# Performance work log

Hardware: AMD Instinct MI355X
Metric: run time of the kernel (lower is better)

Reference implementation:

```python
import jax, jax.numpy as jnp
import numpy as np

N, E, D, H, G, OUT = 50000, 800000, 128, 128, 64, 10


def setup_inputs() -> dict:
    key = jax.random.key(0)
    ks = jax.random.split(key, 10)
    x = jax.random.normal(ks[0], (N, D), dtype=jnp.float32)
    edge_index = jax.random.randint(ks[1], (2, E), 0, N, dtype=jnp.int64)
    batch = jnp.sort(jax.random.randint(ks[2], (N,), 0, G, dtype=jnp.int64))
    s = 1.0 / np.sqrt(D)
    W0 = jax.random.normal(ks[3], (D, H), dtype=jnp.float32) * s
    W1 = jax.random.normal(ks[4], (H, H), dtype=jnp.float32) * s
    W2 = jax.random.normal(ks[5], (H, H), dtype=jnp.float32) * s
    M0w = jax.random.normal(ks[6], (H, H), dtype=jnp.float32) * s
    M0b = jnp.zeros((H,), dtype=jnp.float32)
    M1w = jax.random.normal(ks[7], (H, OUT), dtype=jnp.float32) * s
    M1b = jnp.zeros((OUT,), dtype=jnp.float32)
    return dict(x=x, W0=W0, W1=W1, W2=W2, M0w=M0w, M0b=M0b, M1w=M1w, M1b=M1b,
                edge_index=edge_index, batch=batch)


def gcn_conv(x, W, src, dst):
    # PyG GCNConv (bias=False): h = x @ W; out = D^-1/2 (A + I) D^-1/2 h
    h = x @ W
    deg = jnp.zeros((N,), h.dtype).at[dst].add(1.0) + 1.0  # +1 for self-loop
    dinv = deg ** -0.5
    w = dinv[src] * dinv[dst]  # [E]
    agg = jax.ops.segment_sum(h[src] * w[:, None], dst, num_segments=N)
    return agg + h * (dinv * dinv)[:, None]  # self-loop term


def reference(x, W0, W1, W2, M0w, M0b, M1w, M1b, edge_index, batch):
    src, dst = edge_index[0], edge_index[1]
    h = gcn_conv(x, W0, src, dst)
    h = gcn_conv(jax.nn.relu(h), W1, src, dst)
    h = gcn_conv(jax.nn.relu(h), W2, src, dst)
    # global mean pool over graphs
    sums = jax.ops.segment_sum(h, batch, num_segments=G)
    cnts = jax.ops.segment_sum(jnp.ones((N,), h.dtype), batch, num_segments=G)
    pooled = sums / jnp.maximum(cnts, 1.0)[:, None]
    out = pooled @ M0w + M0b
    out = jax.nn.relu(out) @ M1w + M1b
    return out
```

## Files before the change

### kernel.cpp

```cpp
#include <hip/hip_runtime.h>
#include <hip/hip_fp16.h>

#define NN 50000
#define NE 800000
#define DIM 128
#define NG 64
#define NOUT 10

#define NBKT 391
#define HBLK 256
#define CHUNK ((NE + HBLK - 1) / HBLK)
#define BCAP 2560

#define NPB 16
#define AGB (NN / NPB)

#define WPAD 136
#define PSTR (DIM * WPAD)

typedef __attribute__((ext_vector_type(8))) short short8;
typedef __attribute__((ext_vector_type(8))) _Float16 half8;
typedef __attribute__((ext_vector_type(4))) float float4v;

union S8H8 { short8 s; half8 h; };
union SH { short s; _Float16 h; };

#define PREP_WB 48
#define PREP_NB (PREP_WB + 1)
__global__ __launch_bounds__(256) void prep_kernel(const float* __restrict__ W0,
                                                   const float* __restrict__ W1,
                                                   const float* __restrict__ W2,
                                                   short* __restrict__ wsp,
                                                   const int* __restrict__ batch,
                                                   int* __restrict__ first,
                                                   float* __restrict__ pools,
                                                   int* __restrict__ cnt) {
    int bx = blockIdx.x;
    if (bx < PREP_WB) {
        int w = bx >> 4;
        int sub = bx & 15;
        const float* W = (w == 0) ? W0 : (w == 1) ? W1 : W2;
        short* Wp = wsp + w * PSTR;
        #pragma unroll
        for (int t = 0; t < 4; ++t) {
            int idx = sub * 1024 + t * 256 + threadIdx.x;
            int k = idx >> 7, n = idx & 127;
            int phys = n * WPAD + k;
            SH c;
            c.h = (_Float16)W[idx];
            Wp[phys] = c.s;
        }
    } else {
        int g = threadIdx.x;
        if (g <= NG) {
            int lo = 0, hi = NN;
            while (lo < hi) {
                int mid = (lo + hi) >> 1;
                if (batch[mid] < g) lo = mid + 1; else hi = mid;
            }
            first[g] = lo;
        }
        for (int i = threadIdx.x; i < NG * DIM; i += 256) pools[i] = 0.0f;
        for (int i = threadIdx.x; i < NBKT; i += 256) cnt[i] = 0;
    }
}

__global__ __launch_bounds__(256) void scatter_gemm(const int* __restrict__ ei,
                                                    int* __restrict__ cnt,
                                                    unsigned* __restrict__ ebuf,
                                                    const float* __restrict__ X,
                                                    const short* __restrict__ Wsp,
                                                    __half* __restrict__ Y) {
    __shared__ int h[NBKT];
    int bx = blockIdx.x;
    if (bx < HBLK) {
        for (int i = threadIdx.x; i < NBKT; i += 256) h[i] = 0;
        __syncthreads();
        int lo = bx * CHUNK, hi = min(lo + CHUNK, NE);
        for (int e = lo + threadIdx.x; e < hi; e += 256)
            atomicAdd(&h[ei[NE + e] >> 7], 1);
        __syncthreads();
        for (int i = threadIdx.x; i < NBKT; i += 256) {
            int c = h[i];
            int base = (c > 0) ? atomicAdd(&cnt[i], c) : 0;
            h[i] = i * BCAP + base;
        }
        __syncthreads();
        for (int e = lo + threadIdx.x; e < hi; e += 256) {
            int s = ei[e];
            int d = ei[NE + e];
            int pos = atomicAdd(&h[d >> 7], 1);
            ebuf[pos] = ((unsigned)(d & 127) << 16) | (unsigned)s;
        }
    } else {
        int tid = threadIdx.x;
        int wave = tid >> 6;
        int lane = tid & 63;
        int lm = lane & 15;
        int lq = lane >> 4;
        int row0 = (bx - HBLK) * 64 + wave * 16;
        float4v acc[8];
        #pragma unroll
        for (int i = 0; i < 8; ++i) acc[i] = (float4v){0.f, 0.f, 0.f, 0.f};
        #pragma unroll
        for (int kk = 0; kk < 4; ++kk) {
            int r = min(row0 + lm, NN - 1);
            const float* ap = X + (size_t)r * DIM + kk * 32 + lq * 8;
            float4 xa = *(const float4*)ap;
            float4 xb = *(const float4*)(ap + 4);
            half8 av;
            av[0] = (_Float16)xa.x; av[1] = (_Float16)xa.y;
            av[2] = (_Float16)xa.z; av[3] = (_Float16)xa.w;
            av[4] = (_Float16)xb.x; av[5] = (_Float16)xb.y;
            av[6] = (_Float16)xb.z; av[7] = (_Float16)xb.w;
            const short* bp = Wsp + kk * 32 + lq * 8;
            #pragma unroll
            for (int n0 = 0; n0 < 8; ++n0) {
                S8H8 b;
                b.s = *(const short8*)(bp + (lm * 8 + n0) * WPAD);
                acc[n0] = __builtin_amdgcn_mfma_f32_16x16x32_f16(av, b.h, acc[n0], 0, 0, 0);
            }
        }
        #pragma unroll
        for (int rg = 0; rg < 4; ++rg) {
            int row = row0 + lq * 4 + rg;
            if (row < NN) {
                short8 o;
                #pragma unroll
                for (int j = 0; j < 8; ++j) {
                    SH c;
                    c.h = (_Float16)acc[j][rg];
                    o[j] = c.s;
                }
                *(short8*)((short*)Y + (size_t)row * DIM + lm * 8) = o;
            }
        }
    }
}

__device__ __forceinline__ void local_base_scan(const int* __restrict__ cnt,
                                                int* a , int* ps ,
                                                int* base ) {
    int t = threadIdx.x & 255;
    a[2 * t]     = (2 * t < NBKT)     ? cnt[2 * t]     : 0;
    a[2 * t + 1] = (2 * t + 1 < NBKT) ? cnt[2 * t + 1] : 0;
    __syncthreads();
    int loc = a[2 * t] + a[2 * t + 1];
    ps[t] = loc;
    __syncthreads();
    #pragma unroll
    for (int off = 1; off < 256; off <<= 1) {
        int tv = (t >= off) ? ps[t - off] : 0;
        __syncthreads();
        ps[t] += tv;
        __syncthreads();
    }
    int excl = ps[t] - loc;
    base[2 * t] = excl;
    base[2 * t + 1] = excl + a[2 * t];
    __syncthreads();
}

__global__ __launch_bounds__(256) void build_csr(const unsigned* __restrict__ ebuf,
                                                 const int* __restrict__ cnt,
                                                 int* __restrict__ rowoff,
                                                 int* __restrict__ csr_src,
                                                 float* __restrict__ dinv) {
    __shared__ int a[512];
    __shared__ int ps[256];
    __shared__ int base[512];
    __shared__ int deg[128];
    __shared__ int loff[128];
    int g = blockIdx.x;
    int t = threadIdx.x;
    local_base_scan(cnt, a, ps, base);
    int gbase = base[g];
    int rlo = g * BCAP;
    int rhi = rlo + cnt[g];
    if (t < 128) deg[t] = 0;
    __syncthreads();
    for (int p = rlo + t; p < rhi; p += 256)
        atomicAdd(&deg[ebuf[p] >> 16], 1);
    __syncthreads();
    int v = (t < 128) ? deg[t] : 0;
    if (t < 128) loff[t] = v;
    __syncthreads();
    #pragma unroll
    for (int off = 1; off < 128; off <<= 1) {
        int tv = (t < 128 && t >= off) ? loff[t - off] : 0;
        __syncthreads();
        if (t < 128) loff[t] += tv;
        __syncthreads();
    }
    if (t < 128) {
        int excl = loff[t] - v;
        int node = g * 128 + t;
        if (node < NN) {
            rowoff[node] = gbase + excl;
            dinv[node] = 1.0f / sqrtf((float)v + 1.0f);
        }
        if (node == 0) rowoff[NN] = NE;
        deg[t] = gbase + excl;
    }
    __syncthreads();
    for (int p = rlo + t; p < rhi; p += 256) {
        unsigned pk = ebuf[p];
        int pos = atomicAdd(&deg[pk >> 16], 1);
        csr_src[pos] = (int)(pk & 0xFFFFu);
    }
}

template <bool RELU>
__device__ __forceinline__ void gather_node(const __half* __restrict__ Hc,
                                            const int* __restrict__ rowoff,
                                            const int* __restrict__ csr_src,
                                            const float* __restrict__ dinv,
                                            int i, short8* o) {
    int s = rowoff[i], e = rowoff[i + 1];
    float di = dinv[i];
    short8 qs = *(const short8*)(Hc + (size_t)i * DIM);
    float acc1[8] = {0.f, 0.f, 0.f, 0.f, 0.f, 0.f, 0.f, 0.f};
    int p = s;
    for (; p + 3 < e; p += 4) {
        int u0 = csr_src[p];
        int u1 = csr_src[p + 1];
        int u2 = csr_src[p + 2];
        int u3 = csr_src[p + 3];
        float d0 = dinv[u0], d1 = dinv[u1], d2 = dinv[u2], d3 = dinv[u3];
        short8 q0 = *(const short8*)(Hc + (size_t)u0 * DIM);
        short8 q1 = *(const short8*)(Hc + (size_t)u1 * DIM);
        short8 q2 = *(const short8*)(Hc + (size_t)u2 * DIM);
        short8 q3 = *(const short8*)(Hc + (size_t)u3 * DIM);
        #pragma unroll
        for (int k = 0; k < 8; ++k) {
            acc1[k] = fmaf(d0, __half2float(((const __half*)&q0)[k]), acc1[k]);
            acc1[k] = fmaf(d1, __half2float(((const __half*)&q1)[k]), acc1[k]);
            acc1[k] = fmaf(d2, __half2float(((const __half*)&q2)[k]), acc1[k]);
            acc1[k] = fmaf(d3, __half2float(((const __half*)&q3)[k]), acc1[k]);
        }
    }
    for (; p < e; ++p) {
        int u = csr_src[p];
        float d = dinv[u];
        short8 q = *(const short8*)(Hc + (size_t)u * DIM);
        #pragma unroll
        for (int k = 0; k < 8; ++k)
            acc1[k] = fmaf(d, __half2float(((const __half*)&q)[k]), acc1[k]);
    }
    #pragma unroll
    for (int k = 0; k < 8; ++k) {
        float v = di * fmaf(di, __half2float(((const __half*)&qs)[k]), acc1[k]);
        if (RELU) v = fmaxf(v, 0.0f);
        SH c; c.h = (_Float16)v;
        (*o)[k] = c.s;
    }
}

__global__ __launch_bounds__(256) void agg_gemm(const __half* __restrict__ H,
                                                const short* __restrict__ Wsp,
                                                __half* __restrict__ Y,
                                                const int* __restrict__ rowoff,
                                                const int* __restrict__ csr_src,
                                                const float* __restrict__ dinv) {
    __shared__ short A_s[NPB][WPAD];
    int tid = threadIdx.x;
    int nb = blockIdx.x * NPB;
    {
        int g = tid >> 4;
        int ln = tid & 15;
        short8 o;
        gather_node<true>(H + ln * 8, rowoff, csr_src, dinv, nb + g, &o);
        *(short8*)&A_s[g][ln * 8] = o;
    }
    __syncthreads();
    if (tid >= 64) return;
    int lm = tid & 15;
    int lq = tid >> 4;
    float4v acc[8];
    #pragma unroll
    for (int i = 0; i < 8; ++i) acc[i] = (float4v){0.f, 0.f, 0.f, 0.f};
    #pragma unroll
    for (int kk = 0; kk < 4; ++kk) {
        S8H8 av;
        av.s = *(const short8*)&A_s[lm][kk * 32 + lq * 8];
        const short* bp = Wsp + kk * 32 + lq * 8;
        #pragma unroll
        for (int n0 = 0; n0 < 8; ++n0) {
            S8H8 b;
            b.s = *(const short8*)(bp + (lm * 8 + n0) * WPAD);
            acc[n0] = __builtin_amdgcn_mfma_f32_16x16x32_f16(av.h, b.h, acc[n0], 0, 0, 0);
        }
    }
    #pragma unroll
    for (int rg = 0; rg < 4; ++rg) {
        int row = nb + lq * 4 + rg;
        short8 o;
        #pragma unroll
        for (int j = 0; j < 8; ++j) {
            SH c;
            c.h = (_Float16)acc[j][rg];
            o[j] = c.s;
        }
        *(short8*)((short*)Y + (size_t)row * DIM + lm * 8) = o;
    }
}

__global__ __launch_bounds__(256) void agg_pool(const __half* __restrict__ H,
                                                const int* __restrict__ rowoff,
                                                const int* __restrict__ csr_src,
                                                const float* __restrict__ dinv,
                                                const int* __restrict__ batch,
                                                float* __restrict__ pools) {
    __shared__ short A_s[NPB][WPAD];
    __shared__ int gb[NPB];
    int tid = threadIdx.x;
    int nb = blockIdx.x * NPB;
    if (tid < NPB) gb[tid] = batch[nb + tid];
    {
        int g = tid >> 4;
        int ln = tid & 15;
        short8 o;
        gather_node<false>(H + ln * 8, rowoff, csr_src, dinv, nb + g, &o);
        *(short8*)&A_s[g][ln * 8] = o;
    }
    __syncthreads();
    int c = tid & 127;
    int hf = tid >> 7;
    int r0 = hf * 8;
    float acc = 0.f;
    int cg = gb[r0];
    for (int r = r0; r < r0 + 8; ++r) {
        int g2 = gb[r];
        if (g2 != cg) {
            atomicAdd(&pools[cg * DIM + c], acc);
            acc = 0.f;
            cg = g2;
        }
        SH u;
        u.s = A_s[r][c];
        acc += (float)u.h;
    }
    atomicAdd(&pools[cg * DIM + c], acc);
}

__global__ __launch_bounds__(128) void mlp_kernel(const float* __restrict__ pools,
                                                  const int* __restrict__ first,
                                                  const float* __restrict__ M0w,
                                                  const float* __restrict__ M0b,
                                                  const float* __restrict__ M1w,
                                                  const float* __restrict__ M1b,
                                                  float* __restrict__ out) {
    __shared__ float p[DIM];
    __shared__ float t[DIM];
    int g = blockIdx.x;
    int j = threadIdx.x;
    float cnt = (float)max(first[g + 1] - first[g], 1);
    p[j] = pools[g * DIM + j] / cnt;
    __syncthreads();
    float acc = M0b[j];
    #pragma unroll 8
    for (int k = 0; k < DIM; ++k) acc = fmaf(p[k], M0w[k * DIM + j], acc);
    t[j] = fmaxf(acc, 0.0f);
    __syncthreads();
    if (j < NOUT) {
        float o = M1b[j];
        #pragma unroll 8
        for (int k = 0; k < DIM; ++k) o = fmaf(t[k], M1w[k * NOUT + j], o);
        out[g * NOUT + j] = o;
    }
}

extern "C" void kernel_launch(void* const* d_in, const int* in_sizes, int n_in,
                              void* d_out, int out_size, void* d_ws, size_t ws_size,
                              hipStream_t stream) {
    const float* x   = (const float*)d_in[0];
    const float* W0  = (const float*)d_in[1];
    const float* W1  = (const float*)d_in[2];
    const float* W2  = (const float*)d_in[3];
    const float* M0w = (const float*)d_in[4];
    const float* M0b = (const float*)d_in[5];
    const float* M1w = (const float*)d_in[6];
    const float* M1b = (const float*)d_in[7];
    const int* ei    = (const int*)d_in[8];
    const int* batch = (const int*)d_in[9];
    float* out = (float*)d_out;

    char* ws = (char*)d_ws;
    size_t off = 0;
    auto take = [&](size_t bytes) -> void* {
        void* p = ws + off;
        off = (off + bytes + 255) & ~(size_t)255;
        return p;
    };
    __half* hA   = (__half*)take((size_t)NN * DIM * 2);
    __half* hB   = (__half*)take((size_t)NN * DIM * 2);
    unsigned* ebuf = (unsigned*)take((size_t)NBKT * BCAP * 4);
    int* csr_src = (int*)take((size_t)NE * 4);
    int* cnt     = (int*)take((size_t)NBKT * 4);
    int* rowoff  = (int*)take((size_t)(NN + 1) * 4);
    float* dinv  = (float*)take((size_t)NN * 4);
    int* first   = (int*)take((size_t)(NG + 1) * 4);
    float* pools = (float*)take((size_t)NG * DIM * 4);
    short* wsp   = (short*)take((size_t)3 * PSTR * 2);
    (void)ws_size; (void)in_sizes; (void)n_in; (void)out_size;

    const int GB = (NN + 63) / 64;

    prep_kernel<<<PREP_NB, 256, 0, stream>>>(W0, W1, W2, wsp, batch, first, pools, cnt);
    scatter_gemm<<<HBLK + GB, 256, 0, stream>>>(ei, cnt, ebuf, x, wsp, hA);
    build_csr<<<NBKT, 256, 0, stream>>>(ebuf, cnt, rowoff, csr_src, dinv);

    agg_gemm<<<AGB, 256, 0, stream>>>(hA, wsp + PSTR, hB, rowoff, csr_src, dinv);
    agg_gemm<<<AGB, 256, 0, stream>>>(hB, wsp + 2 * PSTR, hA, rowoff, csr_src, dinv);
    agg_pool<<<AGB, 256, 0, stream>>>(hA, rowoff, csr_src, dinv, batch, pools);

    mlp_kernel<<<NG, 128, 0, stream>>>(pools, first, M0w, M0b, M1w, M1b, out);
}
```

Before: 247.8 us.

## Pre-scale GEMM outputs by dinv and drop per-edge dinv gathers; use 16-bit CSR indices

Node degrees are now counted in the prep kernel with global atomics. Each GEMM epilogue then scales its output rows by deg^-1/2, so the aggregation only sums neighbour rows and applies the destination's deg^-1/2 once. This removes a random dinv load and an FMA per edge and halves csr_src storage to 16-bit indices. Zeroing of deg, pools and cnt moves to a single memset. The risks are 800k global atomics on deg in prep, and 16-bit indices that depend on the source node being packed into the low bits of the bucket (relying on the bucket scheme).

```diff
diff --git a/kernel.cpp b/kernel.cpp
--- a/kernel.cpp
+++ b/kernel.cpp
@@ -26,15 +26,18 @@
 union SH { short s; _Float16 h; };
 
 #define PREP_WB 48
-#define PREP_NB (PREP_WB + 1)
+#define DEGH 128
+#define DCH ((NE + DEGH - 1) / DEGH)
+#define PREP_FB (PREP_WB + DEGH)
+#define PREP_NB (PREP_FB + 1)
 __global__ __launch_bounds__(256) void prep_kernel(const float* __restrict__ W0,
                                                    const float* __restrict__ W1,
                                                    const float* __restrict__ W2,
                                                    short* __restrict__ wsp,
+                                                   const int* __restrict__ ei,
+                                                   int* __restrict__ deg,
                                                    const int* __restrict__ batch,
-                                                   int* __restrict__ first,
-                                                   float* __restrict__ pools,
-                                                   int* __restrict__ cnt) {
+                                                   int* __restrict__ first) {
     int bx = blockIdx.x;
     if (bx < PREP_WB) {
         int w = bx >> 4;
@@ -50,6 +53,11 @@
             c.h = (_Float16)W[idx];
             Wp[phys] = c.s;
         }
+    } else if (bx < PREP_FB) {
+        int b = bx - PREP_WB;
+        int lo = b * DCH, hi = min(lo + DCH, NE);
+        for (int e = lo + threadIdx.x; e < hi; e += 256)
+            atomicAdd(&deg[ei[NE + e]], 1);
     } else {
         int g = threadIdx.x;
         if (g <= NG) {
@@ -60,8 +68,6 @@
             }
             first[g] = lo;
         }
-        for (int i = threadIdx.x; i < NG * DIM; i += 256) pools[i] = 0.0f;
-        for (int i = threadIdx.x; i < NBKT; i += 256) cnt[i] = 0;
     }
 }
 
@@ -70,6 +76,7 @@
                                                     unsigned* __restrict__ ebuf,
                                                     const float* __restrict__ X,
                                                     const short* __restrict__ Wsp,
+                                                    const int* __restrict__ deg,
                                                     __half* __restrict__ Y) {
     __shared__ int h[NBKT];
     int bx = blockIdx.x;
@@ -125,11 +132,12 @@
         for (int rg = 0; rg < 4; ++rg) {
             int row = row0 + lq * 4 + rg;
             if (row < NN) {
+                float ds = 1.0f / sqrtf((float)deg[row] + 1.0f);
                 short8 o;
                 #pragma unroll
                 for (int j = 0; j < 8; ++j) {
                     SH c;
-                    c.h = (_Float16)acc[j][rg];
+                    c.h = (_Float16)(acc[j][rg] * ds);
                     o[j] = c.s;
                 }
                 *(short8*)((short*)Y + (size_t)row * DIM + lm * 8) = o;
@@ -164,12 +172,11 @@
 __global__ __launch_bounds__(256) void build_csr(const unsigned* __restrict__ ebuf,
                                                  const int* __restrict__ cnt,
                                                  int* __restrict__ rowoff,
-                                                 int* __restrict__ csr_src,
-                                                 float* __restrict__ dinv) {
+                                                 unsigned short* __restrict__ csr_src) {
     __shared__ int a[512];
     __shared__ int ps[256];
     __shared__ int base[512];
-    __shared__ int deg[128];
+    __shared__ int dcnt[128];
     __shared__ int loff[128];
     int g = blockIdx.x;
     int t = threadIdx.x;
@@ -177,12 +184,12 @@
     int gbase = base[g];
     int rlo = g * BCAP;
     int rhi = rlo + cnt[g];
-    if (t < 128) deg[t] = 0;
+    if (t < 128) dcnt[t] = 0;
     __syncthreads();
     for (int p = rlo + t; p < rhi; p += 256)
-        atomicAdd(&deg[ebuf[p] >> 16], 1);
-    __syncthreads();
-    int v = (t < 128) ? deg[t] : 0;
+        atomicAdd(&dcnt[ebuf[p] >> 16], 1);
+    __syncthreads();
+    int v = (t < 128) ? dcnt[t] : 0;
     if (t < 128) loff[t] = v;
     __syncthreads();
     #pragma unroll
@@ -195,29 +202,26 @@
     if (t < 128) {
         int excl = loff[t] - v;
         int node = g * 128 + t;
-        if (node < NN) {
-            rowoff[node] = gbase + excl;
-            dinv[node] = 1.0f / sqrtf((float)v + 1.0f);
-        }
+        if (node < NN) rowoff[node] = gbase + excl;
         if (node == 0) rowoff[NN] = NE;
-        deg[t] = gbase + excl;
+        dcnt[t] = gbase + excl;
     }
     __syncthreads();
     for (int p = rlo + t; p < rhi; p += 256) {
         unsigned pk = ebuf[p];
-        int pos = atomicAdd(&deg[pk >> 16], 1);
-        csr_src[pos] = (int)(pk & 0xFFFFu);
+        int pos = atomicAdd(&dcnt[pk >> 16], 1);
+        csr_src[pos] = (unsigned short)(pk & 0xFFFFu);
     }
 }
 
 template <bool RELU>
 __device__ __forceinline__ void gather_node(const __half* __restrict__ Hc,
                                             const int* __restrict__ rowoff,
-                                            const int* __restrict__ csr_src,
-                                            const float* __restrict__ dinv,
+                                            const unsigned short* __restrict__ csr_src,
+                                            const int* __restrict__ deg,
                                             int i, short8* o) {
     int s = rowoff[i], e = rowoff[i + 1];
-    float di = dinv[i];
+    float dv = 1.0f / sqrtf((float)deg[i] + 1.0f);
     short8 qs = *(const short8*)(Hc + (size_t)i * DIM);
     float acc1[8] = {0.f, 0.f, 0.f, 0.f, 0.f, 0.f, 0.f, 0.f};
     int p = s;
@@ -226,30 +230,28 @@
         int u1 = csr_src[p + 1];
         int u2 = csr_src[p + 2];
         int u3 = csr_src[p + 3];
-        float d0 = dinv[u0], d1 = dinv[u1], d2 = dinv[u2], d3 = dinv[u3];
         short8 q0 = *(const short8*)(Hc + (size_t)u0 * DIM);
         short8 q1 = *(const short8*)(Hc + (size_t)u1 * DIM);
         short8 q2 = *(const short8*)(Hc + (size_t)u2 * DIM);
         short8 q3 = *(const short8*)(Hc + (size_t)u3 * DIM);
         #pragma unroll
         for (int k = 0; k < 8; ++k) {
-            acc1[k] = fmaf(d0, __half2float(((const __half*)&q0)[k]), acc1[k]);
-            acc1[k] = fmaf(d1, __half2float(((const __half*)&q1)[k]), acc1[k]);
-            acc1[k] = fmaf(d2, __half2float(((const __half*)&q2)[k]), acc1[k]);
-            acc1[k] = fmaf(d3, __half2float(((const __half*)&q3)[k]), acc1[k]);
+            acc1[k] += __half2float(((const __half*)&q0)[k]);
+            acc1[k] += __half2float(((const __half*)&q1)[k]);
+            acc1[k] += __half2float(((const __half*)&q2)[k]);
+            acc1[k] += __half2float(((const __half*)&q3)[k]);
         }
     }
     for (; p < e; ++p) {
         int u = csr_src[p];
-        float d = dinv[u];
         short8 q = *(const short8*)(Hc + (size_t)u * DIM);
         #pragma unroll
         for (int k = 0; k < 8; ++k)
-            acc1[k] = fmaf(d, __half2float(((const __half*)&q)[k]), acc1[k]);
+            acc1[k] += __half2float(((const __half*)&q)[k]);
     }
     #pragma unroll
     for (int k = 0; k < 8; ++k) {
-        float v = di * fmaf(di, __half2float(((const __half*)&qs)[k]), acc1[k]);
+        float v = dv * (acc1[k] + __half2float(((const __half*)&qs)[k]));
         if (RELU) v = fmaxf(v, 0.0f);
         SH c; c.h = (_Float16)v;
         (*o)[k] = c.s;
@@ -260,8 +262,8 @@
                                                 const short* __restrict__ Wsp,
                                                 __half* __restrict__ Y,
                                                 const int* __restrict__ rowoff,
-                                                const int* __restrict__ csr_src,
-                                                const float* __restrict__ dinv) {
+                                                const unsigned short* __restrict__ csr_src,
+                                                const int* __restrict__ deg) {
     __shared__ short A_s[NPB][WPAD];
     int tid = threadIdx.x;
     int nb = blockIdx.x * NPB;
@@ -269,7 +271,7 @@
         int g = tid >> 4;
         int ln = tid & 15;
         short8 o;
-        gather_node<true>(H + ln * 8, rowoff, csr_src, dinv, nb + g, &o);
+        gather_node<true>(H + ln * 8, rowoff, csr_src, deg, nb + g, &o);
         *(short8*)&A_s[g][ln * 8] = o;
     }
     __syncthreads();
@@ -294,11 +296,12 @@
     #pragma unroll
     for (int rg = 0; rg < 4; ++rg) {
         int row = nb + lq * 4 + rg;
+        float ds = 1.0f / sqrtf((float)deg[row] + 1.0f);
         short8 o;
         #pragma unroll
         for (int j = 0; j < 8; ++j) {
             SH c;
-            c.h = (_Float16)acc[j][rg];
+            c.h = (_Float16)(acc[j][rg] * ds);
             o[j] = c.s;
         }
         *(short8*)((short*)Y + (size_t)row * DIM + lm * 8) = o;
@@ -307,8 +310,8 @@
 
 __global__ __launch_bounds__(256) void agg_pool(const __half* __restrict__ H,
                                                 const int* __restrict__ rowoff,
-                                                const int* __restrict__ csr_src,
-                                                const float* __restrict__ dinv,
+                                                const unsigned short* __restrict__ csr_src,
+                                                const int* __restrict__ deg,
                                                 const int* __restrict__ batch,
                                                 float* __restrict__ pools) {
     __shared__ short A_s[NPB][WPAD];
@@ -320,7 +323,7 @@
         int g = tid >> 4;
         int ln = tid & 15;
         short8 o;
-        gather_node<false>(H + ln * 8, rowoff, csr_src, dinv, nb + g, &o);
+        gather_node<false>(H + ln * 8, rowoff, csr_src, deg, nb + g, &o);
         *(short8*)&A_s[g][ln * 8] = o;
     }
     __syncthreads();
@@ -395,24 +398,27 @@
     __half* hA   = (__half*)take((size_t)NN * DIM * 2);
     __half* hB   = (__half*)take((size_t)NN * DIM * 2);
     unsigned* ebuf = (unsigned*)take((size_t)NBKT * BCAP * 4);
-    int* csr_src = (int*)take((size_t)NE * 4);
+    unsigned short* csr_src = (unsigned short*)take((size_t)NE * 2);
+    int* rowoff  = (int*)take((size_t)(NN + 1) * 4);
+    int* first   = (int*)take((size_t)(NG + 1) * 4);
+    short* wsp   = (short*)take((size_t)3 * PSTR * 2);
+    size_t z0 = off;
+    int* deg     = (int*)take((size_t)NN * 4);
+    float* pools = (float*)take((size_t)NG * DIM * 4);
     int* cnt     = (int*)take((size_t)NBKT * 4);
-    int* rowoff  = (int*)take((size_t)(NN + 1) * 4);
-    float* dinv  = (float*)take((size_t)NN * 4);
-    int* first   = (int*)take((size_t)(NG + 1) * 4);
-    float* pools = (float*)take((size_t)NG * DIM * 4);
-    short* wsp   = (short*)take((size_t)3 * PSTR * 2);
+    size_t zlen = off - z0;
     (void)ws_size; (void)in_sizes; (void)n_in; (void)out_size;
 
     const int GB = (NN + 63) / 64;
 
-    prep_kernel<<<PREP_NB, 256, 0, stream>>>(W0, W1, W2, wsp, batch, first, pools, cnt);
-    scatter_gemm<<<HBLK + GB, 256, 0, stream>>>(ei, cnt, ebuf, x, wsp, hA);
-    build_csr<<<NBKT, 256, 0, stream>>>(ebuf, cnt, rowoff, csr_src, dinv);
-
-    agg_gemm<<<AGB, 256, 0, stream>>>(hA, wsp + PSTR, hB, rowoff, csr_src, dinv);
-    agg_gemm<<<AGB, 256, 0, stream>>>(hB, wsp + 2 * PSTR, hA, rowoff, csr_src, dinv);
-    agg_pool<<<AGB, 256, 0, stream>>>(hA, rowoff, csr_src, dinv, batch, pools);
+    hipMemsetAsync(ws + z0, 0, zlen, stream);
+    prep_kernel<<<PREP_NB, 256, 0, stream>>>(W0, W1, W2, wsp, ei, deg, batch, first);
+    scatter_gemm<<<HBLK + GB, 256, 0, stream>>>(ei, cnt, ebuf, x, wsp, deg, hA);
+    build_csr<<<NBKT, 256, 0, stream>>>(ebuf, cnt, rowoff, csr_src);
+
+    agg_gemm<<<AGB, 256, 0, stream>>>(hA, wsp + PSTR, hB, rowoff, csr_src, deg);
+    agg_gemm<<<AGB, 256, 0, stream>>>(hB, wsp + 2 * PSTR, hA, rowoff, csr_src, deg);
+    agg_pool<<<AGB, 256, 0, stream>>>(hA, rowoff, csr_src, deg, batch, pools);
 
     mlp_kernel<<<NG, 128, 0, stream>>>(pools, first, M0w, M0b, M1w, M1b, out);
 }
```

Result: slower. 278.2 us (+12.2%).
